# Performance work log

Hardware: AMD Instinct MI355X
Metric: run time of the kernel (lower is better)

## Reference

```python
import jax, jax.numpy as jnp
import numpy as np
import math

B, N, DIM, DEPTH, HEADS, DHEAD = 4, 8192, 256, 4, 8, 32
NB = int(DHEAD * math.log(DHEAD))  # 110 random features (performer_pytorch default)
INNER = HEADS * DHEAD  # 256


def _ortho_proj(rng, nb, d):
    # gaussian orthogonal random matrix, scaling=0 (row norms of a fresh gaussian)
    blocks = []
    for _ in range(-(-nb // d)):
        q, _ = np.linalg.qr(rng.standard_normal((d, d)))
        blocks.append(q.T)
    m = np.concatenate(blocks, 0)[:nb]
    mult = np.linalg.norm(rng.standard_normal((nb, d)), axis=1)
    return (mult[:, None] * m).astype(np.float32)


def setup_inputs() -> dict:
    rng = np.random.default_rng(0)
    p = lambda *s: jnp.asarray((rng.standard_normal(s) * 0.02).astype(np.float32))
    return {
        "x": jnp.asarray(rng.standard_normal((B, N, DIM)).astype(np.float32)),
        "proj": jnp.asarray(np.stack([_ortho_proj(rng, NB, DHEAD) for _ in range(DEPTH)])),
        "ln1_g": jnp.ones((DEPTH, DIM), jnp.float32),
        "ln1_b": jnp.zeros((DEPTH, DIM), jnp.float32),
        "Wq": p(DEPTH, DIM, INNER), "bq": jnp.zeros((DEPTH, INNER), jnp.float32),
        "Wk": p(DEPTH, DIM, INNER), "bk": jnp.zeros((DEPTH, INNER), jnp.float32),
        "Wv": p(DEPTH, DIM, INNER), "bv": jnp.zeros((DEPTH, INNER), jnp.float32),
        "Wo": p(DEPTH, INNER, DIM), "bo": jnp.zeros((DEPTH, DIM), jnp.float32),
        "ln2_g": jnp.ones((DEPTH, DIM), jnp.float32),
        "ln2_b": jnp.zeros((DEPTH, DIM), jnp.float32),
        "Wf1": p(DEPTH, DIM, 4 * DIM), "bf1": jnp.zeros((DEPTH, 4 * DIM), jnp.float32),
        "Wf2": p(DEPTH, 4 * DIM, DIM), "bf2": jnp.zeros((DEPTH, DIM), jnp.float32),
    }


def _ln(x, g, b):
    m = jnp.mean(x, axis=-1, keepdims=True)
    v = jnp.var(x, axis=-1, keepdims=True)
    return (x - m) * jax.lax.rsqrt(v + 1e-5) * g + b


def _softmax_kernel(x, proj, is_query, eps=1e-4):
    # FAVOR+ positive softmax-kernel feature map
    dn = x.shape[-1] ** -0.25
    ratio = proj.shape[0] ** -0.5
    xd = jnp.einsum('bhnd,md->bhnm', x * dn, proj)          # [b,h,n,nb]
    diag = jnp.sum(x * x, axis=-1, keepdims=True) * (0.5 * dn * dn)
    if is_query:
        mx = jnp.max(xd, axis=-1, keepdims=True)
    else:
        mx = jnp.max(xd, axis=(-2, -1), keepdims=True)
    mx = jax.lax.stop_gradient(mx)
    return ratio * (jnp.exp(xd - diag - mx) + eps)


def reference(x, proj, ln1_g, ln1_b, Wq, bq, Wk, bk, Wv, bv, Wo, bo,
              ln2_g, ln2_b, Wf1, bf1, Wf2, bf2):
    b, n, _ = x.shape
    h = x
    for i in range(DEPTH):
        # --- PreNorm FAVOR+ self-attention ---
        y = _ln(h, ln1_g[i], ln1_b[i])
        q = (y @ Wq[i] + bq[i]).reshape(b, n, HEADS, DHEAD).transpose(0, 2, 1, 3)
        k = (y @ Wk[i] + bk[i]).reshape(b, n, HEADS, DHEAD).transpose(0, 2, 1, 3)
        v = (y @ Wv[i] + bv[i]).reshape(b, n, HEADS, DHEAD).transpose(0, 2, 1, 3)
        qp = _softmax_kernel(q, proj[i], True)   # [b,h,n,nb]
        kp = _softmax_kernel(k, proj[i], False)  # [b,h,n,nb]
        d_inv = 1.0 / jnp.einsum('bhnm,bhm->bhn', qp, kp.sum(axis=2))
        ctx = jnp.einsum('bhnm,bhnd->bhmd', kp, v)          # [b,h,nb,d]
        o = jnp.einsum('bhnm,bhmd,bhn->bhnd', qp, ctx, d_inv)
        o = o.transpose(0, 2, 1, 3).reshape(b, n, INNER)
        h = h + o @ Wo[i] + bo[i]
        # --- PreNorm FFN ---
        y = _ln(h, ln2_g[i], ln2_b[i])
        h = h + jax.nn.gelu(y @ Wf1[i] + bf1[i]) @ Wf2[i] + bf2[i]
    return h
```

## Files before the change

### kernel.cpp

```cpp
#include <hip/hip_runtime.h>
#include <math.h>

#define NSEQ 8192
#define BATCH 4
#define DIM 256
#define HEADS 8
#define DHEAD 32
#define NB 110
#define INNER 256
#define FFDIM 1024
#define MROWS (BATCH * NSEQ)
#define BH (BATCH * HEADS)

typedef __attribute__((ext_vector_type(8))) short bf16x8;
typedef __attribute__((ext_vector_type(4))) short bf16x4;
typedef __attribute__((ext_vector_type(4))) float f32x4;

typedef __attribute__((address_space(1))) const void* gas_cvp;
typedef __attribute__((address_space(3))) void* las_vp;

constexpr float c_dn = 0.42044820762685725f;
constexpr float c_diagf = 0.08838834764831845f;
constexpr float c_ratio = 0.09534625892455922f;

__device__ __forceinline__ unsigned short f2b(float f) {
    unsigned u = __float_as_uint(f);
    unsigned r = (u + 0x7FFFu + ((u >> 16) & 1u)) >> 16;
    return (unsigned short)r;
}
__device__ __forceinline__ float b2f(unsigned short u) {
    return __uint_as_float((unsigned)u << 16);
}

__global__ __launch_bounds__(256) void cvt_kernel(const float4* __restrict__ src,
                                                  bf16x4* __restrict__ dst, int n4) {
    int i = blockIdx.x * 256 + threadIdx.x;
    if (i < n4) {
        float4 v = src[i];
        bf16x4 o = {(short)f2b(v.x), (short)f2b(v.y), (short)f2b(v.z), (short)f2b(v.w)};
        dst[i] = o;
    }
}
__global__ __launch_bounds__(256) void bcat_kernel(const float* __restrict__ bq,
                                                   const float* __restrict__ bk,
                                                   const float* __restrict__ bv,
                                                   float* __restrict__ out) {
    int l = blockIdx.x, t = threadIdx.x;
    out[l * 768 + t] = bq[l * 256 + t];
    out[l * 768 + 256 + t] = bk[l * 256 + t];
    out[l * 768 + 512 + t] = bv[l * 256 + t];
}

__global__ __launch_bounds__(256) void ln_kernel(const float* __restrict__ x,
                                                 const float* __restrict__ g,
                                                 const float* __restrict__ bta,
                                                 unsigned short* __restrict__ y) {
    int wave = threadIdx.x >> 6, lane = threadIdx.x & 63;
    int row = blockIdx.x * 4 + wave;
    const float* xr = x + (size_t)row * DIM;
    float4 v = *(const float4*)(xr + lane * 4);
    float s = v.x + v.y + v.z + v.w;
    float sq = v.x * v.x + v.y * v.y + v.z * v.z + v.w * v.w;
    #pragma unroll
    for (int off = 32; off; off >>= 1) {
        s += __shfl_xor(s, off);
        sq += __shfl_xor(sq, off);
    }
    float mean = s * (1.0f / DIM);
    float var = sq * (1.0f / DIM) - mean * mean;
    float rstd = rsqrtf(var + 1e-5f);
    float4 gg = *(const float4*)(g + lane * 4);
    float4 bb = *(const float4*)(bta + lane * 4);
    bf16x4 o;
    o[0] = (short)f2b((v.x - mean) * rstd * gg.x + bb.x);
    o[1] = (short)f2b((v.y - mean) * rstd * gg.y + bb.y);
    o[2] = (short)f2b((v.z - mean) * rstd * gg.z + bb.z);
    o[3] = (short)f2b((v.w - mean) * rstd * gg.w + bb.w);
    *(bf16x4*)(y + (size_t)row * DIM + lane * 4) = o;
}

__global__ __launch_bounds__(256) void wt_kernel(const float* __restrict__ in,
                                                 unsigned short* __restrict__ out,
                                                 int K, int Nn, int lstride) {
    __shared__ float t32[32][33];
    int l = blockIdx.z;
    const float* inp = in + (size_t)l * K * Nn;
    unsigned short* outp = out + (size_t)l * lstride;
    int k0 = blockIdx.x * 32, n0 = blockIdx.y * 32;
    int tx = threadIdx.x & 31, ty = threadIdx.x >> 5;
    #pragma unroll
    for (int i = 0; i < 4; ++i)
        t32[ty + i * 8][tx] = inp[(size_t)(k0 + ty + i * 8) * Nn + n0 + tx];
    __syncthreads();
    #pragma unroll
    for (int i = 0; i < 4; ++i) {
        int r = ty + i * 8;
        outp[(size_t)(n0 + r) * K + k0 + tx] = f2b(t32[tx][r]);
    }
}

template <int EPI>
__global__ __launch_bounds__(256) void gemm_mfma(const unsigned short* __restrict__ A,
                                                 const unsigned short* __restrict__ Wt,
                                                 const float* __restrict__ bias,
                                                 void* __restrict__ Cv,
                                                 int Nn, int K) {
    __shared__ __align__(16) unsigned short pool[16384];
    unsigned short* AsP = pool;
    unsigned short* BsP = pool + 8192;
    int tid = threadIdx.x;
    int nwg = gridDim.x * gridDim.y;
    int orig = blockIdx.y * gridDim.x + blockIdx.x;
    int swz = (orig & 7) * (nwg >> 3) + (orig >> 3);
    int m0 = (swz / gridDim.x) * 128, n0 = (swz % gridDim.x) * 128;
    int wave = tid >> 6, lane = tid & 63;
    int wm = (wave >> 1) * 64, wn = (wave & 1) * 64;
    int lr = lane & 15, lg = lane >> 4;
    f32x4 acc[4][4];
    #pragma unroll
    for (int i = 0; i < 4; ++i)
        #pragma unroll
        for (int j = 0; j < 4; ++j) acc[i][j] = (f32x4){0.f, 0.f, 0.f, 0.f};

    int rowS[2], chS[2];
    #pragma unroll
    for (int j = 0; j < 2; ++j) {
        int f = wave * 128 + j * 64 + lane;
        rowS[j] = f >> 2;
        chS[j] = ((f & 3) ^ ((rowS[j] >> 1) & 3)) * 8;
    }
    int rdA[4], rdB[4];
    #pragma unroll
    for (int i = 0; i < 4; ++i) {
        int ra = wm + i * 16 + lr;
        rdA[i] = ra * 32 + (lg ^ ((ra >> 1) & 3)) * 8;
        int rb = wn + i * 16 + lr;
        rdB[i] = rb * 32 + (lg ^ ((rb >> 1) & 3)) * 8;
    }

    const int NT = K >> 5;
    #pragma unroll
    for (int j = 0; j < 2; ++j) {
        const unsigned short* srcA = A + (size_t)(m0 + rowS[j]) * K + chS[j];
        __builtin_amdgcn_global_load_lds((gas_cvp)srcA,
                                         (las_vp)(AsP + wave * 1024 + j * 512), 16, 0, 0);
        const unsigned short* srcB = Wt + (size_t)(n0 + rowS[j]) * K + chS[j];
        __builtin_amdgcn_global_load_lds((gas_cvp)srcB,
                                         (las_vp)(BsP + wave * 1024 + j * 512), 16, 0, 0);
    }
    for (int kt = 0; kt < NT; ++kt) {
        int cur = kt & 1;
        if (kt + 1 < NT) {
            int nxt = cur ^ 1;
            int koff = (kt + 1) * 32;
            #pragma unroll
            for (int j = 0; j < 2; ++j) {
                const unsigned short* srcA = A + (size_t)(m0 + rowS[j]) * K + koff + chS[j];
                __builtin_amdgcn_global_load_lds((gas_cvp)srcA,
                                                 (las_vp)(AsP + nxt * 4096 + wave * 1024 + j * 512), 16, 0, 0);
                const unsigned short* srcB = Wt + (size_t)(n0 + rowS[j]) * K + koff + chS[j];
                __builtin_amdgcn_global_load_lds((gas_cvp)srcB,
                                                 (las_vp)(BsP + nxt * 4096 + wave * 1024 + j * 512), 16, 0, 0);
            }
            asm volatile("s_waitcnt vmcnt(4)" ::: "memory");
        } else {
            asm volatile("s_waitcnt vmcnt(0)" ::: "memory");
        }
        __builtin_amdgcn_s_barrier();
        __builtin_amdgcn_sched_barrier(0);
        bf16x8 af[4], bfv[4];
        #pragma unroll
        for (int i = 0; i < 4; ++i) af[i] = *(bf16x8*)&AsP[cur * 4096 + rdA[i]];
        #pragma unroll
        for (int j = 0; j < 4; ++j) bfv[j] = *(bf16x8*)&BsP[cur * 4096 + rdB[j]];
        #pragma unroll
        for (int i = 0; i < 4; ++i)
            #pragma unroll
            for (int j = 0; j < 4; ++j)
                acc[i][j] = __builtin_amdgcn_mfma_f32_16x16x32_bf16(af[i], bfv[j], acc[i][j], 0, 0, 0);
        __builtin_amdgcn_sched_barrier(0);
        __builtin_amdgcn_s_barrier();
    }

    if (EPI == 2) {
        #pragma unroll
        for (int i = 0; i < 4; ++i) {
            #pragma unroll
            for (int j = 0; j < 4; ++j) {
                int col = n0 + wn + j * 16 + lr;
                float bv = bias[col];
                #pragma unroll
                for (int r = 0; r < 4; ++r) {
                    int row = m0 + wm + i * 16 + lg * 4 + r;
                    float u = acc[i][j][r] + bv;
                    float t = 1.5957691216057308f * (u + 0.044715f * u * u * u);
                    float gv = u / (1.0f + __expf(-t));
                    ((unsigned short*)Cv)[(size_t)row * Nn + col] = f2b(gv);
                }
            }
        }
    } else {
        #pragma unroll
        for (int i = 0; i < 4; ++i) {
            #pragma unroll
            for (int j = 0; j < 4; ++j) {
                int tcol = wn + j * 16 + lr;
                float bv = bias[n0 + tcol];
                #pragma unroll
                for (int r = 0; r < 4; ++r) {
                    int trow = wm + i * 16 + lg * 4 + r;
                    float c = acc[i][j][r] + bv;
                    pool[trow * 128 + (((tcol >> 3) ^ (trow & 7)) << 3) + (tcol & 7)] = f2b(c);
                }
            }
        }
        __syncthreads();
        #pragma unroll
        for (int cch = 0; cch < 8; ++cch) {
            int g = cch * 256 + tid;
            int row = g >> 4, cc = g & 15;
            bf16x8 val = *(bf16x8*)&pool[row * 128 + ((cc ^ (row & 7)) << 3)];
            int grow = m0 + row;
            int gcol = n0 + cc * 8;
            if (EPI == 3) {
                size_t idx = (size_t)(gcol >> 8) * ((size_t)MROWS * DIM) + (size_t)grow * 256 + (gcol & 255);
                *(bf16x8*)((unsigned short*)Cv + idx) = val;
            } else {
                *(bf16x8*)((unsigned short*)Cv + (size_t)grow * Nn + gcol) = val;
            }
        }
    }
}

template <int DO_LN, int F32OUT>
__global__ __launch_bounds__(256) void gemm_ln(const unsigned short* __restrict__ A,
                                               const unsigned short* __restrict__ Wt,
                                               const float* __restrict__ bias,
                                               const unsigned short* __restrict__ res,
                                               void* __restrict__ hout,
                                               unsigned short* __restrict__ yout,
                                               const float* __restrict__ gam,
                                               const float* __restrict__ bet,
                                               int K) {
    __shared__ __align__(16) unsigned short As[2][64 * 32];
    __shared__ __align__(16) unsigned short Bs[2][256 * 32];
    int tid = threadIdx.x;
    int nwg = gridDim.y;
    int orig = blockIdx.y;
    int swz = (orig & 7) * (nwg >> 3) + (orig >> 3);
    int m0 = swz * 64;
    int wave = tid >> 6, lane = tid & 63;
    int lr = lane & 15, lg = lane >> 4;

    f32x4 acc[16];
    #pragma unroll
    for (int j = 0; j < 16; ++j) acc[j] = (f32x4){0.f, 0.f, 0.f, 0.f};

    int fA = wave * 64 + lane;
    int rowA = fA >> 2, chA = ((fA & 3) ^ ((rowA >> 1) & 3)) * 8;
    int rowB[4], chB[4];
    #pragma unroll
    for (int j = 0; j < 4; ++j) {
        int f = wave * 256 + j * 64 + lane;
        rowB[j] = f >> 2;
        chB[j] = ((f & 3) ^ ((rowB[j] >> 1) & 3)) * 8;
    }
    int raA = wave * 16 + lr;
    int rdAo = raA * 32 + (lg ^ ((raA >> 1) & 3)) * 8;
    int rdBo[16];
    #pragma unroll
    for (int j = 0; j < 16; ++j) {
        int rb = j * 16 + lr;
        rdBo[j] = rb * 32 + (lg ^ ((rb >> 1) & 3)) * 8;
    }

    const int NT = K >> 5;
    {
        const unsigned short* srcA = A + (size_t)(m0 + rowA) * K + chA;
        __builtin_amdgcn_global_load_lds((gas_cvp)srcA, (las_vp)(&As[0][wave * 512]), 16, 0, 0);
        #pragma unroll
        for (int j = 0; j < 4; ++j) {
            const unsigned short* srcB = Wt + (size_t)rowB[j] * K + chB[j];
            __builtin_amdgcn_global_load_lds((gas_cvp)srcB, (las_vp)(&Bs[0][wave * 2048 + j * 512]), 16, 0, 0);
        }
    }
    for (int kt = 0; kt < NT; ++kt) {
        int cur = kt & 1;
        if (kt + 1 < NT) {
            int nxt = cur ^ 1;
            int koff = (kt + 1) * 32;
            const unsigned short* srcA = A + (size_t)(m0 + rowA) * K + koff + chA;
            __builtin_amdgcn_global_load_lds((gas_cvp)srcA, (las_vp)(&As[nxt][wave * 512]), 16, 0, 0);
            #pragma unroll
            for (int j = 0; j < 4; ++j) {
                const unsigned short* srcB = Wt + (size_t)rowB[j] * K + koff + chB[j];
                __builtin_amdgcn_global_load_lds((gas_cvp)srcB, (las_vp)(&Bs[nxt][wave * 2048 + j * 512]), 16, 0, 0);
            }
            asm volatile("s_waitcnt vmcnt(5)" ::: "memory");
        } else {
            asm volatile("s_waitcnt vmcnt(0)" ::: "memory");
        }
        __builtin_amdgcn_s_barrier();
        __builtin_amdgcn_sched_barrier(0);
        bf16x8 af = *(bf16x8*)&As[cur][rdAo];
        #pragma unroll
        for (int j = 0; j < 16; ++j) {
            bf16x8 bv = *(bf16x8*)&Bs[cur][rdBo[j]];
            acc[j] = __builtin_amdgcn_mfma_f32_16x16x32_bf16(af, bv, acc[j], 0, 0, 0);
        }
        __builtin_amdgcn_sched_barrier(0);
        __builtin_amdgcn_s_barrier();
    }

    float rs[4] = {0.f, 0.f, 0.f, 0.f};
    float rq[4] = {0.f, 0.f, 0.f, 0.f};
    #pragma unroll
    for (int j = 0; j < 16; ++j) {
        int col = j * 16 + lr;
        float bv = bias[col];
        #pragma unroll
        for (int r = 0; r < 4; ++r) {
            int row = m0 + wave * 16 + lg * 4 + r;
            float c = acc[j][r] + bv + b2f(res[(size_t)row * 256 + col]);
            if (F32OUT) ((float*)hout)[(size_t)row * 256 + col] = c;
            else ((unsigned short*)hout)[(size_t)row * 256 + col] = f2b(c);
            acc[j][r] = c;
            if (DO_LN) { rs[r] += c; rq[r] += c * c; }
        }
    }
    if (DO_LN) {
        #pragma unroll
        for (int r = 0; r < 4; ++r) {
            float s = rs[r], sq = rq[r];
            s += __shfl_xor(s, 1);  sq += __shfl_xor(sq, 1);
            s += __shfl_xor(s, 2);  sq += __shfl_xor(sq, 2);
            s += __shfl_xor(s, 4);  sq += __shfl_xor(sq, 4);
            s += __shfl_xor(s, 8);  sq += __shfl_xor(sq, 8);
            rs[r] = s; rq[r] = sq;
        }
        #pragma unroll
        for (int r = 0; r < 4; ++r) {
            float mean = rs[r] * (1.0f / 256.0f);
            float var = rq[r] * (1.0f / 256.0f) - mean * mean;
            rs[r] = mean;
            rq[r] = rsqrtf(var + 1e-5f);
        }
        #pragma unroll
        for (int j = 0; j < 16; ++j) {
            int col = j * 16 + lr;
            float gv = gam[col], bb = bet[col];
            #pragma unroll
            for (int r = 0; r < 4; ++r) {
                int row = m0 + wave * 16 + lg * 4 + r;
                float yv = (acc[j][r] - rs[r]) * rq[r] * gv + bb;
                yout[(size_t)row * 256 + col] = f2b(yv);
            }
        }
    }
}

__global__ __launch_bounds__(256) void kmaxg_kernel(const unsigned short* __restrict__ k,
                                                    const float* __restrict__ proj,
                                                    float* __restrict__ partial,
                                                    float* __restrict__ ctx) {
    __shared__ unsigned short As[128][40];
    __shared__ unsigned short Pj[112][40];
    __shared__ float wmax[4][8];
    int tid = threadIdx.x;
    int r0 = blockIdx.x * 128;
    if (tid < 96) ctx[blockIdx.x * 96 + tid] = 0.0f;
    for (int idx = tid; idx < 112 * 8; idx += 256) {
        int m = idx >> 3, f4 = idx & 7;
        if (m < NB) {
            float4 va = *(const float4*)(proj + m * 32 + f4 * 4);
            bf16x4 pk = {(short)f2b(va.x), (short)f2b(va.y), (short)f2b(va.z), (short)f2b(va.w)};
            *(bf16x4*)&Pj[m][f4 * 4] = pk;
        } else {
            *(bf16x4*)&Pj[m][f4 * 4] = (bf16x4){0, 0, 0, 0};
        }
    }
    int arow = tid >> 1, ahalf = tid & 1;
    const unsigned short* ap = k + (size_t)(r0 + arow) * 32 + ahalf * 16;
    *(bf16x8*)&As[arow][ahalf * 16] = *(const bf16x8*)ap;
    *(bf16x8*)&As[arow][ahalf * 16 + 8] = *(const bf16x8*)(ap + 8);
    __syncthreads();
    int wave = tid >> 6, lane = tid & 63, lr = lane & 15, lg = lane >> 4;
    float mymax[4] = {-1e30f, -1e30f, -1e30f, -1e30f};
    #pragma unroll
    for (int mt = 0; mt < 2; ++mt) {
        bf16x8 af = *(bf16x8*)&As[(2 * wave + mt) * 16 + lr][lg * 8];
        #pragma unroll
        for (int nt = 0; nt < 7; ++nt) {
            bf16x8 bfp = *(bf16x8*)&Pj[nt * 16 + lr][lg * 8];
            f32x4 d = (f32x4){0.f, 0.f, 0.f, 0.f};
            d = __builtin_amdgcn_mfma_f32_16x16x32_bf16(af, bfp, d, 0, 0, 0);
            if (!(nt == 6 && lr >= 14)) {
                #pragma unroll
                for (int r = 0; r < 4; ++r) mymax[r] = fmaxf(mymax[r], d[r]);
            }
        }
    }
    #pragma unroll
    for (int r = 0; r < 4; ++r) {
        float v = mymax[r];
        v = fmaxf(v, __shfl_xor(v, 1));
        v = fmaxf(v, __shfl_xor(v, 2));
        v = fmaxf(v, __shfl_xor(v, 4));
        v = fmaxf(v, __shfl_xor(v, 8));
        v = fmaxf(v, __shfl_xor(v, 32));
        mymax[r] = v;
    }
    if (lane == 0 || lane == 16) {
        int hb = (lane >> 4) & 1;
        #pragma unroll
        for (int r = 0; r < 4; ++r) wmax[wave][4 * hb + r] = mymax[r];
    }
    __syncthreads();
    if (tid < 8) {
        float m = fmaxf(fmaxf(wmax[0][tid], wmax[1][tid]), fmaxf(wmax[2][tid], wmax[3][tid]));
        partial[blockIdx.x * 8 + tid] = m * c_dn;
    }
}

__global__ __launch_bounds__(256) void ctxg_kernel(const unsigned short* __restrict__ k,
                                                   const unsigned short* __restrict__ v,
                                                   const float* __restrict__ proj,
                                                   const float* __restrict__ partial,
                                                   float* __restrict__ ctx) {
    __shared__ __align__(16) char pool[34816];
    unsigned short (*As)[40] = (unsigned short(*)[40])pool;
    unsigned short (*KpT)[136] = (unsigned short(*)[136])pool;
    __shared__ unsigned short Pj[112][40];
    __shared__ unsigned short VsT[48][136];
    __shared__ float dg[128];
    __shared__ float redbuf[4];
    int tid = threadIdx.x;
    int bh = blockIdx.y, b = bh >> 3, h = bh & 7;
    int n_base = blockIdx.x * 512;
    {
        float m = fmaxf(partial[(size_t)(b * 512 + tid) * 8 + h],
                        partial[(size_t)(b * 512 + 256 + tid) * 8 + h]);
        #pragma unroll
        for (int off = 32; off; off >>= 1) m = fmaxf(m, __shfl_xor(m, off));
        if ((tid & 63) == 0) redbuf[tid >> 6] = m;
    }
    for (int idx = tid; idx < 112 * 8; idx += 256) {
        int m = idx >> 3, f4 = idx & 7;
        if (m < NB) {
            float4 va = *(const float4*)(proj + m * 32 + f4 * 4);
            bf16x4 pk = {(short)f2b(va.x), (short)f2b(va.y), (short)f2b(va.z), (short)f2b(va.w)};
            *(bf16x4*)&Pj[m][f4 * 4] = pk;
        } else {
            *(bf16x4*)&Pj[m][f4 * 4] = (bf16x4){0, 0, 0, 0};
        }
    }
    for (int idx = tid; idx < 16 * 136; idx += 256) KpT[112 + idx / 136][idx % 136] = 0;
    for (int idx = tid; idx < 16 * 128; idx += 256) {
        int rr = 32 + (idx >> 7), nn = idx & 127;
        VsT[rr][nn] = (rr == 32) ? (unsigned short)0x3F80 : (unsigned short)0;
    }
    __syncthreads();
    float mx = fmaxf(fmaxf(redbuf[0], redbuf[1]), fmaxf(redbuf[2], redbuf[3]));
    int wave = tid >> 6, lane = tid & 63, lr = lane & 15, lg = lane >> 4;
    int arow = tid >> 1, ahalf = tid & 1;
    f32x4 ctxacc[2][3];
    #pragma unroll
    for (int mt = 0; mt < 2; ++mt)
        #pragma unroll
        for (int nt = 0; nt < 3; ++nt) ctxacc[mt][nt] = (f32x4){0.f, 0.f, 0.f, 0.f};

    for (int ni = 0; ni < 4; ++ni) {
        int n0 = n_base + ni * 128;
        {
            const unsigned short* kp_ = k + ((size_t)(b * NSEQ + n0 + arow) * 256 + h * 32 + ahalf * 16);
            bf16x8 k0 = *(const bf16x8*)kp_;
            bf16x8 k1 = *(const bf16x8*)(kp_ + 8);
            *(bf16x8*)&As[arow][ahalf * 16] = k0;
            *(bf16x8*)&As[arow][ahalf * 16 + 8] = k1;
            float ssq = 0.f;
            #pragma unroll
            for (int e = 0; e < 8; ++e) {
                float a = b2f((unsigned short)k0[e]), bb = b2f((unsigned short)k1[e]);
                ssq += a * a + bb * bb;
            }
            ssq += __shfl_xor(ssq, 1);
            if (ahalf == 0) dg[arow] = ssq * c_diagf;
        }
        #pragma unroll
        for (int it = 0; it < 4; ++it) {
            int idx = it * 256 + tid;
            int nn = idx >> 3, f4 = idx & 7;
            bf16x4 vv = *(const bf16x4*)(v + ((size_t)(b * NSEQ + n0 + nn) * 256 + h * 32 + f4 * 4));
            VsT[f4 * 4 + 0][nn] = (unsigned short)vv[0];
            VsT[f4 * 4 + 1][nn] = (unsigned short)vv[1];
            VsT[f4 * 4 + 2][nn] = (unsigned short)vv[2];
            VsT[f4 * 4 + 3][nn] = (unsigned short)vv[3];
        }
        __syncthreads();
        f32x4 xds[2][7];
        #pragma unroll
        for (int mt = 0; mt < 2; ++mt) {
            bf16x8 af = *(bf16x8*)&As[(2 * wave + mt) * 16 + lr][lg * 8];
            #pragma unroll
            for (int nt = 0; nt < 7; ++nt) {
                bf16x8 bfp = *(bf16x8*)&Pj[nt * 16 + lr][lg * 8];
                f32x4 d = (f32x4){0.f, 0.f, 0.f, 0.f};
                xds[mt][nt] = __builtin_amdgcn_mfma_f32_16x16x32_bf16(af, bfp, d, 0, 0, 0);
            }
        }
        __syncthreads();
        #pragma unroll
        for (int mt = 0; mt < 2; ++mt)
            #pragma unroll
            for (int nt = 0; nt < 7; ++nt) {
                int m = nt * 16 + lr;
                #pragma unroll
                for (int r = 0; r < 4; ++r) {
                    int nn = (2 * wave + mt) * 16 + lg * 4 + r;
                    float kpv = (m < NB) ? c_ratio * (__expf(xds[mt][nt][r] * c_dn - dg[nn] - mx) + 1e-4f) : 0.f;
                    KpT[m][nn] = f2b(kpv);
                }
            }
        __syncthreads();
        #pragma unroll
        for (int ks = 0; ks < 4; ++ks)
            #pragma unroll
            for (int mt = 0; mt < 2; ++mt) {
                bf16x8 af2 = *(bf16x8*)&KpT[(2 * wave + mt) * 16 + lr][ks * 32 + lg * 8];
                #pragma unroll
                for (int nt = 0; nt < 3; ++nt) {
                    bf16x8 bf2v = *(bf16x8*)&VsT[nt * 16 + lr][ks * 32 + lg * 8];
                    ctxacc[mt][nt] = __builtin_amdgcn_mfma_f32_16x16x32_bf16(af2, bf2v, ctxacc[mt][nt], 0, 0, 0);
                }
            }
        __syncthreads();
    }
    #pragma unroll
    for (int mt = 0; mt < 2; ++mt)
        #pragma unroll
        for (int nt = 0; nt < 3; ++nt)
            #pragma unroll
            for (int r = 0; r < 4; ++r) {
                int m = (2 * wave + mt) * 16 + lg * 4 + r;
                atomicAdd(&ctx[((size_t)bh * 128 + m) * 48 + nt * 16 + lr], ctxacc[mt][nt][r]);
            }
}

__global__ __launch_bounds__(256) void og_kernel(const unsigned short* __restrict__ q,
                                                 const float* __restrict__ proj,
                                                 const float* __restrict__ ctx,
                                                 unsigned short* __restrict__ o) {
    __shared__ __align__(16) char pool[34816];
    unsigned short (*As)[40] = (unsigned short(*)[40])pool;
    unsigned short (*Qp)[136] = (unsigned short(*)[136])pool;
    __shared__ unsigned short Pj[112][40];
    __shared__ unsigned short CsT[48][136];
    __shared__ float dg[128];
    int tid = threadIdx.x;
    int bh = blockIdx.x >> 6, b = bh >> 3, h = bh & 7;
    int n0 = (blockIdx.x & 63) * 128;
    for (int idx = tid; idx < 112 * 8; idx += 256) {
        int m = idx >> 3, f4 = idx & 7;
        if (m < NB) {
            float4 va = *(const float4*)(proj + m * 32 + f4 * 4);
            bf16x4 pk = {(short)f2b(va.x), (short)f2b(va.y), (short)f2b(va.z), (short)f2b(va.w)};
            *(bf16x4*)&Pj[m][f4 * 4] = pk;
        } else {
            *(bf16x4*)&Pj[m][f4 * 4] = (bf16x4){0, 0, 0, 0};
        }
    }
    for (int idx = tid; idx < 128 * 12; idx += 256) {
        int m = idx / 12, c4 = idx - m * 12;
        float4 cv = *(const float4*)(ctx + ((size_t)bh * 128 + m) * 48 + c4 * 4);
        CsT[c4 * 4 + 0][m] = f2b(cv.x);
        CsT[c4 * 4 + 1][m] = f2b(cv.y);
        CsT[c4 * 4 + 2][m] = f2b(cv.z);
        CsT[c4 * 4 + 3][m] = f2b(cv.w);
    }
    int arow = tid >> 1, ahalf = tid & 1;
    {
        const unsigned short* qp_ = q + ((size_t)(b * NSEQ + n0 + arow) * 256 + h * 32 + ahalf * 16);
        bf16x8 q0 = *(const bf16x8*)qp_;
        bf16x8 q1 = *(const bf16x8*)(qp_ + 8);
        *(bf16x8*)&As[arow][ahalf * 16] = q0;
        *(bf16x8*)&As[arow][ahalf * 16 + 8] = q1;
        float ssq = 0.f;
        #pragma unroll
        for (int e = 0; e < 8; ++e) {
            float a = b2f((unsigned short)q0[e]), bb = b2f((unsigned short)q1[e]);
            ssq += a * a + bb * bb;
        }
        ssq += __shfl_xor(ssq, 1);
        if (ahalf == 0) dg[arow] = ssq * c_diagf;
    }
    __syncthreads();
    int wave = tid >> 6, lane = tid & 63, lr = lane & 15, lg = lane >> 4;
    f32x4 xds[2][7];
    #pragma unroll
    for (int mt = 0; mt < 2; ++mt) {
        bf16x8 af = *(bf16x8*)&As[(2 * wave + mt) * 16 + lr][lg * 8];
        #pragma unroll
        for (int nt = 0; nt < 7; ++nt) {
            bf16x8 bfp = *(bf16x8*)&Pj[nt * 16 + lr][lg * 8];
            f32x4 d = (f32x4){0.f, 0.f, 0.f, 0.f};
            xds[mt][nt] = __builtin_amdgcn_mfma_f32_16x16x32_bf16(af, bfp, d, 0, 0, 0);
        }
    }
    float rmax[2][4];
    #pragma unroll
    for (int mt = 0; mt < 2; ++mt)
        #pragma unroll
        for (int r = 0; r < 4; ++r) {
            float mv = -1e30f;
            #pragma unroll
            for (int nt = 0; nt < 7; ++nt)
                if (!(nt == 6 && lr >= 14)) mv = fmaxf(mv, xds[mt][nt][r]);
            mv = fmaxf(mv, __shfl_xor(mv, 1));
            mv = fmaxf(mv, __shfl_xor(mv, 2));
            mv = fmaxf(mv, __shfl_xor(mv, 4));
            mv = fmaxf(mv, __shfl_xor(mv, 8));
            rmax[mt][r] = mv;
        }
    __syncthreads();
    #pragma unroll
    for (int mt = 0; mt < 2; ++mt)
        #pragma unroll
        for (int r = 0; r < 4; ++r) {
            int row = (2 * wave + mt) * 16 + lg * 4 + r;
            #pragma unroll
            for (int nt = 0; nt < 7; ++nt) {
                int m = nt * 16 + lr;
                float qpv = (m < NB)
                    ? c_ratio * (__expf((xds[mt][nt][r] - rmax[mt][r]) * c_dn - dg[row]) + 1e-4f)
                    : 0.f;
                Qp[row][m] = f2b(qpv);
            }
            Qp[row][112 + lr] = 0;
        }
    __syncthreads();
    f32x4 oacc[2][3];
    #pragma unroll
    for (int mt = 0; mt < 2; ++mt)
        #pragma unroll
        for (int nt = 0; nt < 3; ++nt) oacc[mt][nt] = (f32x4){0.f, 0.f, 0.f, 0.f};
    #pragma unroll
    for (int ks = 0; ks < 4; ++ks)
        #pragma unroll
        for (int mt = 0; mt < 2; ++mt) {
            bf16x8 af2 = *(bf16x8*)&Qp[(2 * wave + mt) * 16 + lr][ks * 32 + lg * 8];
            #pragma unroll
            for (int nt = 0; nt < 3; ++nt) {
                bf16x8 bf2v = *(bf16x8*)&CsT[nt * 16 + lr][ks * 32 + lg * 8];
                oacc[mt][nt] = __builtin_amdgcn_mfma_f32_16x16x32_bf16(af2, bf2v, oacc[mt][nt], 0, 0, 0);
            }
        }
    #pragma unroll
    for (int mt = 0; mt < 2; ++mt)
        #pragma unroll
        for (int r = 0; r < 4; ++r) {
            int row = (2 * wave + mt) * 16 + lg * 4 + r;
            int n = n0 + row;
            float den = __shfl(oacc[mt][2][r], lane & 48);
            float inv = 1.0f / den;
            size_t base = (size_t)(b * NSEQ + n) * 256 + h * 32;
            o[base + lr] = f2b(oacc[mt][0][r] * inv);
            o[base + 16 + lr] = f2b(oacc[mt][1][r] * inv);
        }
}

extern "C" void kernel_launch(void* const* d_in, const int* in_sizes, int n_in,
                              void* d_out, int out_size, void* d_ws, size_t ws_size,
                              hipStream_t stream) {
    const float* x = (const float*)d_in[0];
    const float* proj = (const float*)d_in[1];
    const float* ln1_g = (const float*)d_in[2];
    const float* ln1_b = (const float*)d_in[3];
    const float* Wq = (const float*)d_in[4];
    const float* bq = (const float*)d_in[5];
    const float* Wk = (const float*)d_in[6];
    const float* bk = (const float*)d_in[7];
    const float* Wv = (const float*)d_in[8];
    const float* bv = (const float*)d_in[9];
    const float* Wo = (const float*)d_in[10];
    const float* bo = (const float*)d_in[11];
    const float* ln2_g = (const float*)d_in[12];
    const float* ln2_b = (const float*)d_in[13];
    const float* Wf1 = (const float*)d_in[14];
    const float* bf1 = (const float*)d_in[15];
    const float* Wf2 = (const float*)d_in[16];
    const float* bf2 = (const float*)d_in[17];

    float* hf = (float*)d_out;
    const size_t ACT = (size_t)MROWS * DIM;
    unsigned short* y = (unsigned short*)d_ws;
    unsigned short* q = y + ACT;
    unsigned short* k = q + ACT;
    unsigned short* v = k + ACT;
    unsigned short* mid = v + ACT;
    unsigned short* hb = mid + 4 * ACT;
    float* ctx = (float*)(hb + ACT);
    float* partial = ctx + (size_t)BH * 128 * 48;
    float* bqkv = partial + 2048 * 8;
    unsigned short* wt = (unsigned short*)(bqkv + 4 * 768);
    unsigned short* o = y;

    const int WT_L = 786432;

    cvt_kernel<<<(int)(ACT / 4) / 256, 256, 0, stream>>>((const float4*)x, (bf16x4*)hb, (int)(ACT / 4));

    wt_kernel<<<dim3(8, 8, 4), 256, 0, stream>>>(Wq, wt + 0, 256, 256, WT_L);
    wt_kernel<<<dim3(8, 8, 4), 256, 0, stream>>>(Wk, wt + 65536, 256, 256, WT_L);
    wt_kernel<<<dim3(8, 8, 4), 256, 0, stream>>>(Wv, wt + 131072, 256, 256, WT_L);
    wt_kernel<<<dim3(8, 8, 4), 256, 0, stream>>>(Wo, wt + 196608, 256, 256, WT_L);
    wt_kernel<<<dim3(8, 32, 4), 256, 0, stream>>>(Wf1, wt + 262144, 256, 1024, WT_L);
    wt_kernel<<<dim3(32, 8, 4), 256, 0, stream>>>(Wf2, wt + 524288, 1024, 256, WT_L);
    bcat_kernel<<<4, 256, 0, stream>>>(bq, bk, bv, bqkv);

    ln_kernel<<<MROWS / 4, 256, 0, stream>>>(x, ln1_g, ln1_b, y);

    for (int i = 0; i < 4; ++i) {
        const float* proj_i = proj + (size_t)i * NB * DHEAD;
        const unsigned short* wl = wt + (size_t)i * WT_L;
        gemm_mfma<3><<<dim3(6, 256), 256, 0, stream>>>(y, wl + 0, bqkv + i * 768, q, 768, DIM);

        kmaxg_kernel<<<2048, 256, 0, stream>>>(k, proj_i, partial, ctx);
        ctxg_kernel<<<dim3(16, BH), 256, 0, stream>>>(k, v, proj_i, partial, ctx);
        og_kernel<<<BH * 64, 256, 0, stream>>>(q, proj_i, ctx, o);

        gemm_ln<1, 0><<<dim3(1, MROWS / 64), 256, 0, stream>>>(o, wl + 196608, bo + i * DIM, hb, hb, y,
                                                               ln2_g + i * DIM, ln2_b + i * DIM, INNER);

        gemm_mfma<2><<<dim3(8, 256), 256, 0, stream>>>(y, wl + 262144, bf1 + i * FFDIM, mid, FFDIM, DIM);
        if (i < 3) {
            gemm_ln<1, 0><<<dim3(1, MROWS / 64), 256, 0, stream>>>(mid, wl + 524288, bf2 + i * DIM, hb, hb, y,
                                                                   ln1_g + (i + 1) * DIM, ln1_b + (i + 1) * DIM, FFDIM);
        } else {
            gemm_ln<0, 1><<<dim3(1, MROWS / 64), 256, 0, stream>>>(mid, wl + 524288, bf2 + i * DIM, hb, hf, nullptr,
                                                                   nullptr, nullptr, FFDIM);
        }
    }
}
```

Measured before the change: 757.6 us.

## Use 2x2 wave tiling in gemm_ln and double ctxg grid parallelism

gemm_ln previously had each wave compute 16 rows across all 256 columns, loading one A fragment and 16 B fragments per k-step. It now splits the 64x256 tile into 2x2 wave quadrants of 32x128, loading 2 A and 8 B fragments per k-step, which cuts LDS reads per MFMA. Because each row's LayerNorm statistics are now split across two waves, a shared-memory reduction and an extra __syncthreads are added. Separately, ctxg_kernel now covers 256 sequence positions per block instead of 512, with twice as many blocks, to raise parallelism at the cost of more atomic or partial accumulation into ctx.

```diff
diff --git a/kernel.cpp b/kernel.cpp
--- a/kernel.cpp
+++ b/kernel.cpp
@@ -244,17 +244,21 @@
                                                int K) {
     __shared__ __align__(16) unsigned short As[2][64 * 32];
     __shared__ __align__(16) unsigned short Bs[2][256 * 32];
+    __shared__ float lnred[64][4];
     int tid = threadIdx.x;
     int nwg = gridDim.y;
     int orig = blockIdx.y;
     int swz = (orig & 7) * (nwg >> 3) + (orig >> 3);
     int m0 = swz * 64;
     int wave = tid >> 6, lane = tid & 63;
+    int wr = wave >> 1, wc = wave & 1;
     int lr = lane & 15, lg = lane >> 4;
 
-    f32x4 acc[16];
-    #pragma unroll
-    for (int j = 0; j < 16; ++j) acc[j] = (f32x4){0.f, 0.f, 0.f, 0.f};
+    f32x4 acc[2][8];
+    #pragma unroll
+    for (int i = 0; i < 2; ++i)
+        #pragma unroll
+        for (int j = 0; j < 8; ++j) acc[i][j] = (f32x4){0.f, 0.f, 0.f, 0.f};
 
     int fA = wave * 64 + lane;
     int rowA = fA >> 2, chA = ((fA & 3) ^ ((rowA >> 1) & 3)) * 8;
@@ -265,12 +269,16 @@
         rowB[j] = f >> 2;
         chB[j] = ((f & 3) ^ ((rowB[j] >> 1) & 3)) * 8;
     }
-    int raA = wave * 16 + lr;
-    int rdAo = raA * 32 + (lg ^ ((raA >> 1) & 3)) * 8;
-    int rdBo[16];
-    #pragma unroll
-    for (int j = 0; j < 16; ++j) {
-        int rb = j * 16 + lr;
+    int rdAo[2];
+    #pragma unroll
+    for (int i = 0; i < 2; ++i) {
+        int ra = wr * 32 + i * 16 + lr;
+        rdAo[i] = ra * 32 + (lg ^ ((ra >> 1) & 3)) * 8;
+    }
+    int rdBo[8];
+    #pragma unroll
+    for (int j = 0; j < 8; ++j) {
+        int rb = wc * 128 + j * 16 + lr;
         rdBo[j] = rb * 32 + (lg ^ ((rb >> 1) & 3)) * 8;
     }
 
@@ -302,58 +310,90 @@
         }
         __builtin_amdgcn_s_barrier();
         __builtin_amdgcn_sched_barrier(0);
-        bf16x8 af = *(bf16x8*)&As[cur][rdAo];
-        #pragma unroll
-        for (int j = 0; j < 16; ++j) {
-            bf16x8 bv = *(bf16x8*)&Bs[cur][rdBo[j]];
-            acc[j] = __builtin_amdgcn_mfma_f32_16x16x32_bf16(af, bv, acc[j], 0, 0, 0);
-        }
+        bf16x8 af[2], bv[8];
+        #pragma unroll
+        for (int i = 0; i < 2; ++i) af[i] = *(bf16x8*)&As[cur][rdAo[i]];
+        #pragma unroll
+        for (int j = 0; j < 8; ++j) bv[j] = *(bf16x8*)&Bs[cur][rdBo[j]];
+        #pragma unroll
+        for (int i = 0; i < 2; ++i)
+            #pragma unroll
+            for (int j = 0; j < 8; ++j)
+                acc[i][j] = __builtin_amdgcn_mfma_f32_16x16x32_bf16(af[i], bv[j], acc[i][j], 0, 0, 0);
         __builtin_amdgcn_sched_barrier(0);
         __builtin_amdgcn_s_barrier();
     }
 
-    float rs[4] = {0.f, 0.f, 0.f, 0.f};
-    float rq[4] = {0.f, 0.f, 0.f, 0.f};
-    #pragma unroll
-    for (int j = 0; j < 16; ++j) {
-        int col = j * 16 + lr;
-        float bv = bias[col];
-        #pragma unroll
-        for (int r = 0; r < 4; ++r) {
-            int row = m0 + wave * 16 + lg * 4 + r;
-            float c = acc[j][r] + bv + b2f(res[(size_t)row * 256 + col]);
-            if (F32OUT) ((float*)hout)[(size_t)row * 256 + col] = c;
-            else ((unsigned short*)hout)[(size_t)row * 256 + col] = f2b(c);
-            acc[j][r] = c;
-            if (DO_LN) { rs[r] += c; rq[r] += c * c; }
+    float rs[2][4], rq[2][4];
+    #pragma unroll
+    for (int i = 0; i < 2; ++i)
+        #pragma unroll
+        for (int r = 0; r < 4; ++r) { rs[i][r] = 0.f; rq[i][r] = 0.f; }
+    #pragma unroll
+    for (int i = 0; i < 2; ++i) {
+        #pragma unroll
+        for (int j = 0; j < 8; ++j) {
+            int col = wc * 128 + j * 16 + lr;
+            float bv = bias[col];
+            #pragma unroll
+            for (int r = 0; r < 4; ++r) {
+                int row = m0 + wr * 32 + i * 16 + lg * 4 + r;
+                float c = acc[i][j][r] + bv + b2f(res[(size_t)row * 256 + col]);
+                if (F32OUT) ((float*)hout)[(size_t)row * 256 + col] = c;
+                else ((unsigned short*)hout)[(size_t)row * 256 + col] = f2b(c);
+                acc[i][j][r] = c;
+                if (DO_LN) { rs[i][r] += c; rq[i][r] += c * c; }
+            }
         }
     }
     if (DO_LN) {
         #pragma unroll
-        for (int r = 0; r < 4; ++r) {
-            float s = rs[r], sq = rq[r];
-            s += __shfl_xor(s, 1);  sq += __shfl_xor(sq, 1);
-            s += __shfl_xor(s, 2);  sq += __shfl_xor(sq, 2);
-            s += __shfl_xor(s, 4);  sq += __shfl_xor(sq, 4);
-            s += __shfl_xor(s, 8);  sq += __shfl_xor(sq, 8);
-            rs[r] = s; rq[r] = sq;
-        }
-        #pragma unroll
-        for (int r = 0; r < 4; ++r) {
-            float mean = rs[r] * (1.0f / 256.0f);
-            float var = rq[r] * (1.0f / 256.0f) - mean * mean;
-            rs[r] = mean;
-            rq[r] = rsqrtf(var + 1e-5f);
-        }
-        #pragma unroll
-        for (int j = 0; j < 16; ++j) {
-            int col = j * 16 + lr;
-            float gv = gam[col], bb = bet[col];
+        for (int i = 0; i < 2; ++i)
             #pragma unroll
             for (int r = 0; r < 4; ++r) {
-                int row = m0 + wave * 16 + lg * 4 + r;
-                float yv = (acc[j][r] - rs[r]) * rq[r] * gv + bb;
-                yout[(size_t)row * 256 + col] = f2b(yv);
+                float s = rs[i][r], sq = rq[i][r];
+                s += __shfl_xor(s, 1);  sq += __shfl_xor(sq, 1);
+                s += __shfl_xor(s, 2);  sq += __shfl_xor(sq, 2);
+                s += __shfl_xor(s, 4);  sq += __shfl_xor(sq, 4);
+                s += __shfl_xor(s, 8);  sq += __shfl_xor(sq, 8);
+                rs[i][r] = s; rq[i][r] = sq;
+            }
+        if (lr == 0) {
+            #pragma unroll
+            for (int i = 0; i < 2; ++i)
+                #pragma unroll
+                for (int r = 0; r < 4; ++r) {
+                    int rl = wr * 32 + i * 16 + lg * 4 + r;
+                    lnred[rl][wc * 2] = rs[i][r];
+                    lnred[rl][wc * 2 + 1] = rq[i][r];
+                }
+        }
+        __syncthreads();
+        float meanv[2][4], rstdv[2][4];
+        #pragma unroll
+        for (int i = 0; i < 2; ++i)
+            #pragma unroll
+            for (int r = 0; r < 4; ++r) {
+                int rl = wr * 32 + i * 16 + lg * 4 + r;
+                float s = lnred[rl][0] + lnred[rl][2];
+                float sq = lnred[rl][1] + lnred[rl][3];
+                float mean = s * (1.0f / 256.0f);
+                float var = sq * (1.0f / 256.0f) - mean * mean;
+                meanv[i][r] = mean;
+                rstdv[i][r] = rsqrtf(var + 1e-5f);
+            }
+        #pragma unroll
+        for (int i = 0; i < 2; ++i) {
+            #pragma unroll
+            for (int j = 0; j < 8; ++j) {
+                int col = wc * 128 + j * 16 + lr;
+                float gv = gam[col], bb = bet[col];
+                #pragma unroll
+                for (int r = 0; r < 4; ++r) {
+                    int row = m0 + wr * 32 + i * 16 + lg * 4 + r;
+                    float yv = (acc[i][j][r] - meanv[i][r]) * rstdv[i][r] * gv + bb;
+                    yout[(size_t)row * 256 + col] = f2b(yv);
+                }
             }
         }
     }
@@ -436,7 +476,7 @@
     __shared__ float redbuf[4];
     int tid = threadIdx.x;
     int bh = blockIdx.y, b = bh >> 3, h = bh & 7;
-    int n_base = blockIdx.x * 512;
+    int n_base = blockIdx.x * 256;
     {
         float m = fmaxf(partial[(size_t)(b * 512 + tid) * 8 + h],
                         partial[(size_t)(b * 512 + 256 + tid) * 8 + h]);
@@ -469,7 +509,7 @@
         #pragma unroll
         for (int nt = 0; nt < 3; ++nt) ctxacc[mt][nt] = (f32x4){0.f, 0.f, 0.f, 0.f};
 
-    for (int ni = 0; ni < 4; ++ni) {
+    for (int ni = 0; ni < 2; ++ni) {
         int n0 = n_base + ni * 128;
         {
             const unsigned short* kp_ = k + ((size_t)(b * NSEQ + n0 + arow) * 256 + h * 32 + ahalf * 16);
@@ -724,7 +764,7 @@
         gemm_mfma<3><<<dim3(6, 256), 256, 0, stream>>>(y, wl + 0, bqkv + i * 768, q, 768, DIM);
 
         kmaxg_kernel<<<2048, 256, 0, stream>>>(k, proj_i, partial, ctx);
-        ctxg_kernel<<<dim3(16, BH), 256, 0, stream>>>(k, v, proj_i, partial, ctx);
+        ctxg_kernel<<<dim3(32, BH), 256, 0, stream>>>(k, v, proj_i, partial, ctx);
         og_kernel<<<BH * 64, 256, 0, stream>>>(q, proj_i, ctx, o);
 
         gemm_ln<1, 0><<<dim3(1, MROWS / 64), 256, 0, stream>>>(o, wl + 196608, bo + i * DIM, hb, hb, y,
```

After: 789.9 us. 4.3% more time.
